# Kernel optimization log

Hardware: AMD Instinct MI355X
Metric: run time of the kernel (lower is better)

## Reference

```python
import jax, jax.numpy as jnp
import numpy as np

NUM_HEADS = 16

def setup_inputs() -> dict:
    key = jax.random.key(0)
    ks = jax.random.split(key, 9)
    B, S, H = 16, 512, 1024
    hidden_states = jax.random.normal(ks[0], (B, S, H), dtype=jnp.float32)
    attention_mask = jax.random.randint(ks[1], (B, 1, S, S), 0, 2, dtype=jnp.int32)
    group_prob = jax.random.uniform(ks[2], (B, S, S), dtype=jnp.float32)
    scale = 0.02
    Wq = jax.random.normal(ks[3], (H, H), dtype=jnp.float32) * scale
    bq = jnp.zeros((H,), dtype=jnp.float32)
    Wk = jax.random.normal(ks[4], (H, H), dtype=jnp.float32) * scale
    bk = jnp.zeros((H,), dtype=jnp.float32)
    Wv = jax.random.normal(ks[5], (H, H), dtype=jnp.float32) * scale
    bv = jnp.zeros((H,), dtype=jnp.float32)
    return {"hidden_states": hidden_states, "attention_mask": attention_mask,
            "group_prob": group_prob, "Wq": Wq, "bq": bq, "Wk": Wk, "bk": bk,
            "Wv": Wv, "bv": bv}

def reference(hidden_states, attention_mask, group_prob, Wq, bq, Wk, bk, Wv, bv):
    B, S, H = hidden_states.shape
    nh = NUM_HEADS
    dh = H // nh
    # QKV projections (nn.Linear applies x @ W.T + b), split heads -> [B, nh, S, dh]
    def proj(W, b):
        return (hidden_states @ W.T + b).reshape(B, S, nh, dh).transpose(0, 2, 1, 3)
    q = proj(Wq, bq)
    k = proj(Wk, bk)
    v = proj(Wv, bv)
    scores = jnp.einsum('bhqd,bhkd->bhqk', q, k) / jnp.sqrt(jnp.float32(dh))
    # mode 'L': mask where (attention_mask | diag) == 0; diagonal always kept
    diag = jnp.eye(S, dtype=jnp.int32)
    keep = (attention_mask.astype(jnp.int32) | diag) != 0  # [B,1,S,S]
    scores = jnp.where(keep, scores, -jnp.inf)
    probs = jax.nn.softmax(scores, axis=-1)
    probs = probs * group_prob[:, None, :, :]  # group_prob.unsqueeze(1)
    # dropout prob = 0 (eval); head_mask is None
    ctx = jnp.einsum('bhqk,bhkd->bhqd', probs, v)
    ctx = ctx.transpose(0, 2, 1, 3).reshape(B, S, H)
    return (ctx, scores)
```

## Files before the change

### kernel.cpp

```cpp
#include <hip/hip_runtime.h>
#include <cmath>


typedef __bf16 bf16x8 __attribute__((ext_vector_type(8)));
typedef float  f32x4  __attribute__((ext_vector_type(4)));

#define MFMA(a, b, c) __builtin_amdgcn_mfma_f32_16x16x32_bf16(a, b, c, 0, 0, 0)
#define NEG_BIG (-1e30f)

static __device__ __forceinline__ unsigned pk_hi(float a, float b) {
    return (__float_as_uint(a) >> 16) | (__float_as_uint(b) & 0xFFFF0000u);
}
static __device__ __forceinline__ float trf(float x) {
    return __uint_as_float(__float_as_uint(x) & 0xFFFF0000u);
}
static __device__ __forceinline__ unsigned rne16(float x) {
    unsigned b = __float_as_uint(x);
    return (b + 0x7FFFu + ((b >> 16) & 1u)) >> 16;
}
static __device__ __forceinline__ ushort hi16(float x) {
    return (ushort)(__float_as_uint(x) >> 16);
}
static __device__ __forceinline__ bf16x8 ldfrag(const ushort* base, int row, int grp) {
    return *(const bf16x8*)(base + (((row << 3) + (grp ^ (row & 7))) << 3));
}
static __device__ __forceinline__ void gl_lds16(const ushort* g, ushort* l) {
    __builtin_amdgcn_global_load_lds(
        (const __attribute__((address_space(1))) void*)g,
        (__attribute__((address_space(3))) void*)l, 16, 0, 0);
}

__global__ __launch_bounds__(256) void split_planes(
    const float* __restrict__ in, ushort* __restrict__ oh,
    ushort* __restrict__ ol, int n8)
{
    for (int i = blockIdx.x * 256 + threadIdx.x; i < n8; i += gridDim.x * 256) {
        float4 f0 = ((const float4*)in)[2 * i], f1 = ((const float4*)in)[2 * i + 1];
        uint4 hv, lv;
        hv.x = pk_hi(f0.x, f0.y); hv.y = pk_hi(f0.z, f0.w);
        hv.z = pk_hi(f1.x, f1.y); hv.w = pk_hi(f1.z, f1.w);
        lv.x = rne16(f0.x - trf(f0.x)) | (rne16(f0.y - trf(f0.y)) << 16);
        lv.y = rne16(f0.z - trf(f0.z)) | (rne16(f0.w - trf(f0.w)) << 16);
        lv.z = rne16(f1.x - trf(f1.x)) | (rne16(f1.y - trf(f1.y)) << 16);
        lv.w = rne16(f1.z - trf(f1.z)) | (rne16(f1.w - trf(f1.w)) << 16);
        ((uint4*)oh)[i] = hv;
        ((uint4*)ol)[i] = lv;
    }
}

__global__ __launch_bounds__(256, 3) void qkv_mfma(
    const ushort* __restrict__ xh, const ushort* __restrict__ xl,
    const ushort* __restrict__ wh, const ushort* __restrict__ wl,
    const float* __restrict__ bias, ushort* __restrict__ oh, ushort* __restrict__ ol)
{
    __shared__ __align__(16) ushort As[8192], Bs[8192];
    const int n0 = blockIdx.x * 128, m0 = blockIdx.y * 128;
    const int t = threadIdx.x, w = t >> 6, lane = t & 63;
    const int quad = lane >> 4, l15 = lane & 15;
    const int wr = w >> 1, wc = w & 1;

    const f32x4 zero = {0.f, 0.f, 0.f, 0.f};
    f32x4 acc[4][4];
#pragma unroll
    for (int i = 0; i < 4; ++i)
#pragma unroll
        for (int j = 0; j < 4; ++j) acc[i][j] = zero;

    for (int kc = 0; kc < 1024; kc += 32) {
        __syncthreads();
#pragma unroll
        for (int rep = 0; rep < 8; ++rep) {
            int slot = t + (rep & 3) * 256;
            int r = slot >> 3, gs = slot & 7;
            int g = gs ^ (r & 7);
            int kg = g & 3;
            if (rep < 4) {
                const ushort* base = (g & 4) ? xl : xh;
                gl_lds16(base + (size_t)(m0 + r) * 1024 + kc + kg * 8,
                         &As[((rep & 3) * 256 + w * 64) * 8]);
            } else {
                const ushort* base = (g & 4) ? wl : wh;
                gl_lds16(base + (size_t)(n0 + r) * 1024 + kc + kg * 8,
                         &Bs[((rep & 3) * 256 + w * 64) * 8]);
            }
        }
        __syncthreads();
        bf16x8 ah[4], al4[4], bh4[4], bl4[4];
#pragma unroll
        for (int i = 0; i < 4; ++i) {
            int row = wr * 64 + i * 16 + l15;
            ah[i]  = ldfrag(As, row, quad);
            al4[i] = ldfrag(As, row, 4 + quad);
        }
#pragma unroll
        for (int j = 0; j < 4; ++j) {
            int row = wc * 64 + j * 16 + l15;
            bh4[j] = ldfrag(Bs, row, quad);
            bl4[j] = ldfrag(Bs, row, 4 + quad);
        }
#pragma unroll
        for (int i = 0; i < 4; ++i)
#pragma unroll
            for (int j = 0; j < 4; ++j) {
                acc[i][j] = MFMA(ah[i],  bh4[j], acc[i][j]);
                acc[i][j] = MFMA(ah[i],  bl4[j], acc[i][j]);
                acc[i][j] = MFMA(al4[i], bh4[j], acc[i][j]);
            }
    }
#pragma unroll
    for (int j = 0; j < 4; ++j) {
        int n = n0 + wc * 64 + j * 16 + l15;
        float bb = bias[n];
        int h = n >> 6, dd = n & 63;
#pragma unroll
        for (int i = 0; i < 4; ++i)
#pragma unroll
            for (int reg = 0; reg < 4; ++reg) {
                int m = m0 + wr * 64 + i * 16 + quad * 4 + reg;
                int b = m >> 9, s = m & 511;
                float c = acc[i][j][reg] + bb;
                size_t o = (((size_t)(b * 16 + h)) * 512 + s) * 64 + dd;
                oh[o] = hi16(c);
                ol[o] = (ushort)rne16(c - trf(c));
            }
    }
}

__global__ __launch_bounds__(256, 2) void vtrans(
    const ushort* __restrict__ vh, const ushort* __restrict__ vl,
    ushort* __restrict__ vth, ushort* __restrict__ vtl)
{
    __shared__ __align__(16) ushort Th[64 * 72], Tl[64 * 72];
    const int bh = blockIdx.y, s0 = blockIdx.x * 64;
    const int t = threadIdx.x;
#pragma unroll
    for (int rep = 0; rep < 2; ++rep) {
        int slot = t + rep * 256;
        int g = slot >> 6, r = slot & 63;
        size_t src = ((size_t)bh * 512 + s0 + r) * 64 + g * 8;
        uint4 hv = *(const uint4*)&vh[src];
        uint4 lv = *(const uint4*)&vl[src];
        unsigned ha[4] = {hv.x, hv.y, hv.z, hv.w};
        unsigned la[4] = {lv.x, lv.y, lv.z, lv.w};
#pragma unroll
        for (int e = 0; e < 4; ++e) {
            int dd = g * 8 + e * 2;
            Th[dd * 72 + r]       = (ushort)(ha[e] & 0xFFFFu);
            Th[(dd + 1) * 72 + r] = (ushort)(ha[e] >> 16);
            Tl[dd * 72 + r]       = (ushort)(la[e] & 0xFFFFu);
            Tl[(dd + 1) * 72 + r] = (ushort)(la[e] >> 16);
        }
    }
    __syncthreads();
#pragma unroll
    for (int rep = 0; rep < 2; ++rep) {
        int slot = t + rep * 256;
        int dd = slot >> 3, g2 = slot & 7;
        size_t dst = ((size_t)bh * 64 + dd) * 512 + s0 + g2 * 8;
        *(uint4*)&vth[dst] = *(const uint4*)&Th[dd * 72 + g2 * 8];
        *(uint4*)&vtl[dst] = *(const uint4*)&Tl[dd * 72 + g2 * 8];
    }
}

__global__ __launch_bounds__(256, 3) void attn_fused(
    const ushort* __restrict__ qh, const ushort* __restrict__ ql,
    const ushort* __restrict__ kh, const ushort* __restrict__ kl,
    const ushort* __restrict__ vth, const ushort* __restrict__ vtl,
    const int* __restrict__ mask, const float* __restrict__ gp,
    float* __restrict__ sc, float* __restrict__ ctx)
{
    __shared__ __align__(16) ushort Kh[4096], Kl[4096], Vh[4096], Vl[4096];
    __shared__ __align__(16) ushort Ph[4 * 16 * 72], Pl[4 * 16 * 72];

    const int bh = blockIdx.y, b = bh >> 4, h = bh & 15;
    const int q0 = blockIdx.x * 64;
    const int t = threadIdx.x, w = t >> 6, lane = t & 63;
    const int quad = lane >> 4, l15 = lane & 15;

#pragma unroll
    for (int rep = 0; rep < 2; ++rep) {
        int slot = t + rep * 256;
        int r = slot >> 3, gs = slot & 7, g = gs ^ (r & 7);
        size_t src = ((size_t)bh * 512 + q0 + r) * 64 + g * 8;
        gl_lds16(&qh[src], &Kh[(rep * 256 + w * 64) * 8]);
        gl_lds16(&ql[src], &Kl[(rep * 256 + w * 64) * 8]);
    }
    __syncthreads();
    bf16x8 qfh[2], qfl[2];
    {
        int qrow = w * 16 + l15;
#pragma unroll
        for (int ks = 0; ks < 2; ++ks) {
            qfh[ks] = ldfrag(Kh, qrow, ks * 4 + quad);
            qfl[ks] = ldfrag(Kl, qrow, ks * 4 + quad);
        }
    }

    float m_run[4] = {-INFINITY, -INFINITY, -INFINITY, -INFINITY};
    float l_run[4] = {0.f, 0.f, 0.f, 0.f};
    const f32x4 zero = {0.f, 0.f, 0.f, 0.f};
    f32x4 accO[4];
#pragma unroll
    for (int d = 0; d < 4; ++d) accO[d] = zero;

    ushort* phb = Ph + w * 16 * 72;
    ushort* plb = Pl + w * 16 * 72;
    int rowg[4];
#pragma unroll
    for (int reg = 0; reg < 4; ++reg) rowg[reg] = q0 + w * 16 + quad * 4 + reg;

    for (int c = 0; c < 8; ++c) {
        __syncthreads();
#pragma unroll
        for (int rep = 0; rep < 2; ++rep) {
            int slot = t + rep * 256;
            int r = slot >> 3, gs = slot & 7, g = gs ^ (r & 7);
            size_t ks_ = ((size_t)bh * 512 + c * 64 + r) * 64 + g * 8;
            size_t vs_ = ((size_t)bh * 64 + r) * 512 + c * 64 + g * 8;
            int db = (rep * 256 + w * 64) * 8;
            gl_lds16(&kh[ks_],  &Kh[db]);
            gl_lds16(&kl[ks_],  &Kl[db]);
            gl_lds16(&vth[vs_], &Vh[db]);
            gl_lds16(&vtl[vs_], &Vl[db]);
        }
        __syncthreads();

        float sv[4][4];
#pragma unroll
        for (int nt = 0; nt < 4; ++nt) {
            f32x4 a = zero;
#pragma unroll
            for (int ks = 0; ks < 2; ++ks) {
                int krow = nt * 16 + l15;
                bf16x8 kfh = ldfrag(Kh, krow, ks * 4 + quad);
                bf16x8 kfl = ldfrag(Kl, krow, ks * 4 + quad);
                a = MFMA(qfh[ks], kfh, a);
                a = MFMA(qfh[ks], kfl, a);
                a = MFMA(qfl[ks], kfh, a);
            }
            int col = c * 64 + nt * 16 + l15;
#pragma unroll
            for (int reg = 0; reg < 4; ++reg) {
                int row = rowg[reg];
                int mv = mask[(size_t)b * 262144 + (size_t)row * 512 + col];
                float x = a[reg] * 0.125f;
                float val = (mv | (row == col)) ? x : NEG_BIG;
                sc[(size_t)bh * 262144 + (size_t)row * 512 + col] = val;
                sv[nt][reg] = val;
            }
        }
        float alpha[4];
#pragma unroll
        for (int reg = 0; reg < 4; ++reg) {
            float cm = fmaxf(fmaxf(sv[0][reg], sv[1][reg]), fmaxf(sv[2][reg], sv[3][reg]));
            cm = fmaxf(cm, __shfl_xor(cm, 1));
            cm = fmaxf(cm, __shfl_xor(cm, 2));
            cm = fmaxf(cm, __shfl_xor(cm, 4));
            cm = fmaxf(cm, __shfl_xor(cm, 8));
            float mn = fmaxf(m_run[reg], cm);
            alpha[reg] = __expf(m_run[reg] - mn);
            m_run[reg] = mn;
            float rs = 0.f;
#pragma unroll
            for (int nt = 0; nt < 4; ++nt) {
                float e = (sv[nt][reg] > -5e29f) ? __expf(sv[nt][reg] - mn) : 0.f;
                sv[nt][reg] = e;
                rs += e;
            }
            rs += __shfl_xor(rs, 1);
            rs += __shfl_xor(rs, 2);
            rs += __shfl_xor(rs, 4);
            rs += __shfl_xor(rs, 8);
            l_run[reg] = l_run[reg] * alpha[reg] + rs;
        }
#pragma unroll
        for (int nt = 0; nt < 4; ++nt) {
            int col = c * 64 + nt * 16 + l15;
#pragma unroll
            for (int reg = 0; reg < 4; ++reg) {
                float g = gp[(size_t)b * 262144 + (size_t)rowg[reg] * 512 + col];
                float pv = sv[nt][reg] * g;
                int a_ = (quad * 4 + reg) * 72 + nt * 16 + l15;
                phb[a_] = hi16(pv);
                plb[a_] = (ushort)rne16(pv - trf(pv));
            }
        }
#pragma unroll
        for (int d = 0; d < 4; ++d)
#pragma unroll
            for (int reg = 0; reg < 4; ++reg) accO[d][reg] *= alpha[reg];
#pragma unroll
        for (int ks = 0; ks < 2; ++ks) {
            bf16x8 pfh = *(const bf16x8*)&phb[l15 * 72 + ks * 32 + quad * 8];
            bf16x8 pfl = *(const bf16x8*)&plb[l15 * 72 + ks * 32 + quad * 8];
#pragma unroll
            for (int d = 0; d < 4; ++d) {
                bf16x8 vfh = ldfrag(Vh, d * 16 + l15, ks * 4 + quad);
                bf16x8 vfl = ldfrag(Vl, d * 16 + l15, ks * 4 + quad);
                accO[d] = MFMA(pfh, vfh, accO[d]);
                accO[d] = MFMA(pfh, vfl, accO[d]);
                accO[d] = MFMA(pfl, vfh, accO[d]);
            }
        }
    }
#pragma unroll
    for (int reg = 0; reg < 4; ++reg) {
        float inv = 1.f / l_run[reg];
#pragma unroll
        for (int d = 0; d < 4; ++d)
            ctx[((size_t)b * 512 + rowg[reg]) * 1024 + h * 64 + d * 16 + l15] =
                accO[d][reg] * inv;
    }
}

extern "C" void kernel_launch(void* const* d_in, const int* in_sizes, int n_in,
                              void* d_out, int out_size, void* d_ws, size_t ws_size,
                              hipStream_t stream) {
    const float* hs   = (const float*)d_in[0];
    const int*   mask = (const int*)d_in[1];
    const float* gp   = (const float*)d_in[2];
    const float* Wq   = (const float*)d_in[3];
    const float* bq   = (const float*)d_in[4];
    const float* Wk   = (const float*)d_in[5];
    const float* bk   = (const float*)d_in[6];
    const float* Wv   = (const float*)d_in[7];
    const float* bv   = (const float*)d_in[8];

    float* out = (float*)d_out;
    float* ctx = out;
    float* sc  = out + (size_t)16 * 512 * 1024;

    const size_t PL = (size_t)16 * 16 * 512 * 64;
    const size_t WN = (size_t)1024 * 1024;

    ushort* qhp  = (ushort*)d_ws;
    ushort* qlp  = qhp + PL;
    ushort* khp  = qlp + PL;
    ushort* klp  = khp + PL;
    ushort* vthp = klp + PL;
    ushort* vtlp = vthp + PL;

    ushort* scr = (ushort*)sc;
    ushort* xh  = scr;
    ushort* xl  = xh + PL;
    ushort* wqh = xl + PL;
    ushort* wql = wqh + WN;
    ushort* wkh = wql + WN;
    ushort* wkl = wkh + WN;
    ushort* wvh = wkl + WN;
    ushort* wvl = wvh + WN;
    ushort* vhp = wvl + WN;
    ushort* vlp = vhp + PL;

    dim3 blk(256);
    split_planes<<<dim3(2048), blk, 0, stream>>>(hs, xh, xl, (int)(PL / 8));
    split_planes<<<dim3(512),  blk, 0, stream>>>(Wq, wqh, wql, (int)(WN / 8));
    split_planes<<<dim3(512),  blk, 0, stream>>>(Wk, wkh, wkl, (int)(WN / 8));
    split_planes<<<dim3(512),  blk, 0, stream>>>(Wv, wvh, wvl, (int)(WN / 8));
    qkv_mfma<<<dim3(8, 64), blk, 0, stream>>>(xh, xl, wqh, wql, bq, qhp, qlp);
    qkv_mfma<<<dim3(8, 64), blk, 0, stream>>>(xh, xl, wkh, wkl, bk, khp, klp);
    qkv_mfma<<<dim3(8, 64), blk, 0, stream>>>(xh, xl, wvh, wvl, bv, vhp, vlp);
    vtrans<<<dim3(8, 256), blk, 0, stream>>>(vhp, vlp, vthp, vtlp);
    attn_fused<<<dim3(8, 256), blk, 0, stream>>>(qhp, qlp, khp, klp, vthp, vtlp,
                                                 mask, gp, sc, ctx);
}
```

Baseline: 869.4 us.

## Fuse QKV GEMMs into one launch, write V transposed, load K/V directly

Merges the three QKV projection launches into a single grid of 24x64 blocks with a remapped block order, and has the V section write its output already transposed, which removes the separate vtrans kernel. The attention kernel drops LDS staging of Q, K and V and their barriers. It reads MFMA fragments straight from global memory, shrinks LDS to the P buffer and raises the occupancy hint to 4. This cuts launches, one V round-trip and the syncs, but replaces coalesced shared tile loads with per-lane global fragment loads that every wave repeats, relying on cache hits.

```diff
diff --git a/kernel.cpp b/kernel.cpp
--- a/kernel.cpp
+++ b/kernel.cpp
@@ -7,6 +7,8 @@
 
 #define MFMA(a, b, c) __builtin_amdgcn_mfma_f32_16x16x32_bf16(a, b, c, 0, 0, 0)
 #define NEG_BIG (-1e30f)
+#define PL ((size_t)8388608)
+#define WN ((size_t)1048576)
 
 static __device__ __forceinline__ unsigned pk_hi(float a, float b) {
     return (__float_as_uint(a) >> 16) | (__float_as_uint(b) & 0xFFFF0000u);
@@ -48,13 +50,23 @@
     }
 }
 
-__global__ __launch_bounds__(256, 3) void qkv_mfma(
+__global__ __launch_bounds__(256, 3) void qkv3_mfma(
     const ushort* __restrict__ xh, const ushort* __restrict__ xl,
-    const ushort* __restrict__ wh, const ushort* __restrict__ wl,
-    const float* __restrict__ bias, ushort* __restrict__ oh, ushort* __restrict__ ol)
+    const ushort* __restrict__ wall,
+    const float* __restrict__ bq, const float* __restrict__ bk,
+    const float* __restrict__ bv,
+    ushort* __restrict__ qkout, ushort* __restrict__ vth, ushort* __restrict__ vtl)
 {
     __shared__ __align__(16) ushort As[8192], Bs[8192];
-    const int n0 = blockIdx.x * 128, m0 = blockIdx.y * 128;
+    const int lin = blockIdx.y * 24 + blockIdx.x;
+    const int nl = (lin & 7) * 192 + (lin >> 3);
+    const int bx = nl % 24, by = nl / 24;
+    const int sec = bx >> 3, nx = bx & 7;
+    const int n0 = nx * 128, m0 = by * 128;
+    const ushort* wh = wall + (size_t)sec * 2 * WN;
+    const ushort* wl = wh + WN;
+    const float* bias = (sec == 0) ? bq : (sec == 1) ? bk : bv;
+
     const int t = threadIdx.x, w = t >> 6, lane = t & 63;
     const int quad = lane >> 4, l15 = lane & 15;
     const int wr = w >> 1, wc = w & 1;
@@ -107,92 +119,77 @@
                 acc[i][j] = MFMA(al4[i], bh4[j], acc[i][j]);
             }
     }
-#pragma unroll
-    for (int j = 0; j < 4; ++j) {
-        int n = n0 + wc * 64 + j * 16 + l15;
-        float bb = bias[n];
-        int h = n >> 6, dd = n & 63;
-#pragma unroll
-        for (int i = 0; i < 4; ++i)
-#pragma unroll
-            for (int reg = 0; reg < 4; ++reg) {
-                int m = m0 + wr * 64 + i * 16 + quad * 4 + reg;
+
+    if (sec < 2) {
+        ushort* oh = qkout + (size_t)sec * 2 * PL;
+        ushort* ol = oh + PL;
+#pragma unroll
+        for (int j = 0; j < 4; ++j) {
+            int n = n0 + wc * 64 + j * 16 + l15;
+            float bb = bias[n];
+            int h = n >> 6, dd = n & 63;
+#pragma unroll
+            for (int i = 0; i < 4; ++i)
+#pragma unroll
+                for (int reg = 0; reg < 4; ++reg) {
+                    int m = m0 + wr * 64 + i * 16 + quad * 4 + reg;
+                    int b = m >> 9, s = m & 511;
+                    float c = acc[i][j][reg] + bb;
+                    size_t o = (((size_t)(b * 16 + h)) * 512 + s) * 64 + dd;
+                    oh[o] = hi16(c);
+                    ol[o] = (ushort)rne16(c - trf(c));
+                }
+        }
+    } else {
+#pragma unroll
+        for (int j = 0; j < 4; ++j) {
+            int n = n0 + wc * 64 + j * 16 + l15;
+            float bb = bias[n];
+            int h = n >> 6, dd = n & 63;
+#pragma unroll
+            for (int i = 0; i < 4; ++i) {
+                int m = m0 + wr * 64 + i * 16 + quad * 4;
                 int b = m >> 9, s = m & 511;
-                float c = acc[i][j][reg] + bb;
-                size_t o = (((size_t)(b * 16 + h)) * 512 + s) * 64 + dd;
-                oh[o] = hi16(c);
-                ol[o] = (ushort)rne16(c - trf(c));
-            }
-    }
-}
-
-__global__ __launch_bounds__(256, 2) void vtrans(
-    const ushort* __restrict__ vh, const ushort* __restrict__ vl,
-    ushort* __restrict__ vth, ushort* __restrict__ vtl)
-{
-    __shared__ __align__(16) ushort Th[64 * 72], Tl[64 * 72];
-    const int bh = blockIdx.y, s0 = blockIdx.x * 64;
-    const int t = threadIdx.x;
-#pragma unroll
-    for (int rep = 0; rep < 2; ++rep) {
-        int slot = t + rep * 256;
-        int g = slot >> 6, r = slot & 63;
-        size_t src = ((size_t)bh * 512 + s0 + r) * 64 + g * 8;
-        uint4 hv = *(const uint4*)&vh[src];
-        uint4 lv = *(const uint4*)&vl[src];
-        unsigned ha[4] = {hv.x, hv.y, hv.z, hv.w};
-        unsigned la[4] = {lv.x, lv.y, lv.z, lv.w};
-#pragma unroll
-        for (int e = 0; e < 4; ++e) {
-            int dd = g * 8 + e * 2;
-            Th[dd * 72 + r]       = (ushort)(ha[e] & 0xFFFFu);
-            Th[(dd + 1) * 72 + r] = (ushort)(ha[e] >> 16);
-            Tl[dd * 72 + r]       = (ushort)(la[e] & 0xFFFFu);
-            Tl[(dd + 1) * 72 + r] = (ushort)(la[e] >> 16);
-        }
-    }
-    __syncthreads();
-#pragma unroll
-    for (int rep = 0; rep < 2; ++rep) {
-        int slot = t + rep * 256;
-        int dd = slot >> 3, g2 = slot & 7;
-        size_t dst = ((size_t)bh * 64 + dd) * 512 + s0 + g2 * 8;
-        *(uint4*)&vth[dst] = *(const uint4*)&Th[dd * 72 + g2 * 8];
-        *(uint4*)&vtl[dst] = *(const uint4*)&Tl[dd * 72 + g2 * 8];
-    }
-}
-
-__global__ __launch_bounds__(256, 3) void attn_fused(
+                float c0 = acc[i][j][0] + bb, c1 = acc[i][j][1] + bb;
+                float c2 = acc[i][j][2] + bb, c3 = acc[i][j][3] + bb;
+                ushort4 hv, lv;
+                hv.x = hi16(c0); hv.y = hi16(c1); hv.z = hi16(c2); hv.w = hi16(c3);
+                lv.x = (ushort)rne16(c0 - trf(c0));
+                lv.y = (ushort)rne16(c1 - trf(c1));
+                lv.z = (ushort)rne16(c2 - trf(c2));
+                lv.w = (ushort)rne16(c3 - trf(c3));
+                size_t o = (((size_t)(b * 16 + h)) * 64 + dd) * 512 + s;
+                *(ushort4*)&vth[o] = hv;
+                *(ushort4*)&vtl[o] = lv;
+            }
+        }
+    }
+}
+
+__global__ __launch_bounds__(256, 4) void attn_fused(
     const ushort* __restrict__ qh, const ushort* __restrict__ ql,
     const ushort* __restrict__ kh, const ushort* __restrict__ kl,
     const ushort* __restrict__ vth, const ushort* __restrict__ vtl,
     const int* __restrict__ mask, const float* __restrict__ gp,
     float* __restrict__ sc, float* __restrict__ ctx)
 {
-    __shared__ __align__(16) ushort Kh[4096], Kl[4096], Vh[4096], Vl[4096];
-    __shared__ __align__(16) ushort Ph[4 * 16 * 72], Pl[4 * 16 * 72];
+    __shared__ __align__(16) ushort P[9216];
 
     const int bh = blockIdx.y, b = bh >> 4, h = bh & 15;
     const int q0 = blockIdx.x * 64;
     const int t = threadIdx.x, w = t >> 6, lane = t & 63;
     const int quad = lane >> 4, l15 = lane & 15;
 
-#pragma unroll
-    for (int rep = 0; rep < 2; ++rep) {
-        int slot = t + rep * 256;
-        int r = slot >> 3, gs = slot & 7, g = gs ^ (r & 7);
-        size_t src = ((size_t)bh * 512 + q0 + r) * 64 + g * 8;
-        gl_lds16(&qh[src], &Kh[(rep * 256 + w * 64) * 8]);
-        gl_lds16(&ql[src], &Kl[(rep * 256 + w * 64) * 8]);
-    }
-    __syncthreads();
+    ushort* phb = P + w * 2304;
+    ushort* plb = phb + 1152;
+
     bf16x8 qfh[2], qfl[2];
     {
-        int qrow = w * 16 + l15;
+        size_t qoff = ((size_t)bh * 512 + q0 + w * 16 + l15) * 64 + quad * 8;
 #pragma unroll
         for (int ks = 0; ks < 2; ++ks) {
-            qfh[ks] = ldfrag(Kh, qrow, ks * 4 + quad);
-            qfl[ks] = ldfrag(Kl, qrow, ks * 4 + quad);
+            qfh[ks] = *(const bf16x8*)(qh + qoff + ks * 32);
+            qfl[ks] = *(const bf16x8*)(ql + qoff + ks * 32);
         }
     }
 
@@ -203,37 +200,25 @@
 #pragma unroll
     for (int d = 0; d < 4; ++d) accO[d] = zero;
 
-    ushort* phb = Ph + w * 16 * 72;
-    ushort* plb = Pl + w * 16 * 72;
     int rowg[4];
 #pragma unroll
     for (int reg = 0; reg < 4; ++reg) rowg[reg] = q0 + w * 16 + quad * 4 + reg;
 
+    const size_t kbase = (size_t)bh * 512 * 64;
+    const size_t vbase = (size_t)bh * 64 * 512;
+    const size_t mrow = (size_t)b * 262144;
+    const size_t srow = (size_t)bh * 262144;
+
     for (int c = 0; c < 8; ++c) {
-        __syncthreads();
-#pragma unroll
-        for (int rep = 0; rep < 2; ++rep) {
-            int slot = t + rep * 256;
-            int r = slot >> 3, gs = slot & 7, g = gs ^ (r & 7);
-            size_t ks_ = ((size_t)bh * 512 + c * 64 + r) * 64 + g * 8;
-            size_t vs_ = ((size_t)bh * 64 + r) * 512 + c * 64 + g * 8;
-            int db = (rep * 256 + w * 64) * 8;
-            gl_lds16(&kh[ks_],  &Kh[db]);
-            gl_lds16(&kl[ks_],  &Kl[db]);
-            gl_lds16(&vth[vs_], &Vh[db]);
-            gl_lds16(&vtl[vs_], &Vl[db]);
-        }
-        __syncthreads();
-
         float sv[4][4];
 #pragma unroll
         for (int nt = 0; nt < 4; ++nt) {
+            size_t koff = kbase + (size_t)(c * 64 + nt * 16 + l15) * 64 + quad * 8;
             f32x4 a = zero;
 #pragma unroll
             for (int ks = 0; ks < 2; ++ks) {
-                int krow = nt * 16 + l15;
-                bf16x8 kfh = ldfrag(Kh, krow, ks * 4 + quad);
-                bf16x8 kfl = ldfrag(Kl, krow, ks * 4 + quad);
+                bf16x8 kfh = *(const bf16x8*)(kh + koff + ks * 32);
+                bf16x8 kfl = *(const bf16x8*)(kl + koff + ks * 32);
                 a = MFMA(qfh[ks], kfh, a);
                 a = MFMA(qfh[ks], kfl, a);
                 a = MFMA(qfl[ks], kfh, a);
@@ -242,10 +227,10 @@
 #pragma unroll
             for (int reg = 0; reg < 4; ++reg) {
                 int row = rowg[reg];
-                int mv = mask[(size_t)b * 262144 + (size_t)row * 512 + col];
+                int mv = mask[mrow + (size_t)row * 512 + col];
                 float x = a[reg] * 0.125f;
                 float val = (mv | (row == col)) ? x : NEG_BIG;
-                sc[(size_t)bh * 262144 + (size_t)row * 512 + col] = val;
+                sc[srow + (size_t)row * 512 + col] = val;
                 sv[nt][reg] = val;
             }
         }
@@ -278,7 +263,7 @@
             int col = c * 64 + nt * 16 + l15;
 #pragma unroll
             for (int reg = 0; reg < 4; ++reg) {
-                float g = gp[(size_t)b * 262144 + (size_t)rowg[reg] * 512 + col];
+                float g = gp[mrow + (size_t)rowg[reg] * 512 + col];
                 float pv = sv[nt][reg] * g;
                 int a_ = (quad * 4 + reg) * 72 + nt * 16 + l15;
                 phb[a_] = hi16(pv);
@@ -295,8 +280,10 @@
             bf16x8 pfl = *(const bf16x8*)&plb[l15 * 72 + ks * 32 + quad * 8];
 #pragma unroll
             for (int d = 0; d < 4; ++d) {
-                bf16x8 vfh = ldfrag(Vh, d * 16 + l15, ks * 4 + quad);
-                bf16x8 vfl = ldfrag(Vl, d * 16 + l15, ks * 4 + quad);
+                size_t voff = vbase + (size_t)(d * 16 + l15) * 512
+                            + c * 64 + ks * 32 + quad * 8;
+                bf16x8 vfh = *(const bf16x8*)(vth + voff);
+                bf16x8 vfl = *(const bf16x8*)(vtl + voff);
                 accO[d] = MFMA(pfh, vfh, accO[d]);
                 accO[d] = MFMA(pfh, vfl, accO[d]);
                 accO[d] = MFMA(pfl, vfh, accO[d]);
@@ -330,37 +317,25 @@
     float* ctx = out;
     float* sc  = out + (size_t)16 * 512 * 1024;
 
-    const size_t PL = (size_t)16 * 16 * 512 * 64;
-    const size_t WN = (size_t)1024 * 1024;
-
-    ushort* qhp  = (ushort*)d_ws;
-    ushort* qlp  = qhp + PL;
-    ushort* khp  = qlp + PL;
-    ushort* klp  = khp + PL;
-    ushort* vthp = klp + PL;
-    ushort* vtlp = vthp + PL;
-
-    ushort* scr = (ushort*)sc;
-    ushort* xh  = scr;
-    ushort* xl  = xh + PL;
-    ushort* wqh = xl + PL;
-    ushort* wql = wqh + WN;
-    ushort* wkh = wql + WN;
-    ushort* wkl = wkh + WN;
-    ushort* wvh = wkl + WN;
-    ushort* wvl = wvh + WN;
-    ushort* vhp = wvl + WN;
-    ushort* vlp = vhp + PL;
+    ushort* qkout = (ushort*)d_ws;
+    ushort* qhp   = qkout;
+    ushort* qlp   = qhp + PL;
+    ushort* khp   = qlp + PL;
+    ushort* klp   = khp + PL;
+    ushort* vthp  = klp + PL;
+    ushort* vtlp  = vthp + PL;
+
+    ushort* xh   = (ushort*)sc;
+    ushort* xl   = xh + PL;
+    ushort* wall = xl + PL;
 
     dim3 blk(256);
     split_planes<<<dim3(2048), blk, 0, stream>>>(hs, xh, xl, (int)(PL / 8));
-    split_planes<<<dim3(512),  blk, 0, stream>>>(Wq, wqh, wql, (int)(WN / 8));
-    split_planes<<<dim3(512),  blk, 0, stream>>>(Wk, wkh, wkl, (int)(WN / 8));
-    split_planes<<<dim3(512),  blk, 0, stream>>>(Wv, wvh, wvl, (int)(WN / 8));
-    qkv_mfma<<<dim3(8, 64), blk, 0, stream>>>(xh, xl, wqh, wql, bq, qhp, qlp);
-    qkv_mfma<<<dim3(8, 64), blk, 0, stream>>>(xh, xl, wkh, wkl, bk, khp, klp);
-    qkv_mfma<<<dim3(8, 64), blk, 0, stream>>>(xh, xl, wvh, wvl, bv, vhp, vlp);
-    vtrans<<<dim3(8, 256), blk, 0, stream>>>(vhp, vlp, vthp, vtlp);
+    split_planes<<<dim3(512),  blk, 0, stream>>>(Wq, wall + 0 * WN, wall + 1 * WN, (int)(WN / 8));
+    split_planes<<<dim3(512),  blk, 0, stream>>>(Wk, wall + 2 * WN, wall + 3 * WN, (int)(WN / 8));
+    split_planes<<<dim3(512),  blk, 0, stream>>>(Wv, wall + 4 * WN, wall + 5 * WN, (int)(WN / 8));
+    qkv3_mfma<<<dim3(24, 64), blk, 0, stream>>>(xh, xl, wall, bq, bk, bv,
+                                                qkout, vthp, vtlp);
     attn_fused<<<dim3(8, 256), blk, 0, stream>>>(qhp, qlp, khp, klp, vthp, vtlp,
                                                  mask, gp, sc, ctx);
 }
```

Result: slower. 975.2 us (+12.2%).
